# Performance work log

Hardware: AMD Instinct MI355X
Metric: run time of the kernel (lower is better)

The kernel has to match this reference:

```python
import jax, jax.numpy as jnp
import numpy as np

B, IN_CHAN, L = 16, 16, 4096
OUTC, KS = 64, 7

def _conv1d(x, w, b, stride=1, pad=0):
    # x: (N, Cin, L), w: (Cout, Cin, K)
    y = jax.lax.conv_general_dilated(x, w, (stride,), [(pad, pad)],
                                     dimension_numbers=('NCH', 'OIH', 'NCH'))
    return y + b[None, :, None]

def setup_inputs() -> dict:
    key = jax.random.key(0)
    ks = jax.random.split(key, 7)
    x = jax.random.normal(ks[0], (B, 1, L, IN_CHAN), dtype=jnp.float32)
    # offset-predicting conv (inc=1 -> KS offsets), k=3 pad=1
    p_w = jax.random.normal(ks[1], (KS, 1, 3), dtype=jnp.float32) * 0.1
    p_b = jax.random.normal(ks[2], (KS,), dtype=jnp.float32) * 0.1
    # modulation conv (inc=1 -> KS masks), k=3 pad=1
    m_w = jax.random.normal(ks[3], (KS, 1, 3), dtype=jnp.float32) * 0.1
    m_b = jax.random.normal(ks[4], (KS,), dtype=jnp.float32) * 0.1
    # main conv over resampled signal: (1 -> OUTC), k=KS, stride=KS
    c_w = jax.random.normal(ks[5], (OUTC, 1, KS), dtype=jnp.float32) * (1.0 / np.sqrt(KS))
    c_b = jax.random.normal(ks[6], (OUTC,), dtype=jnp.float32) * 0.1
    return {"x": x, "p_w": p_w, "p_b": p_b, "m_w": m_w, "m_b": m_b,
            "c_w": c_w, "c_b": c_b}

def _deform_conv1d(xs, p_w, p_b, m_w, m_b, c_w, c_b):
    # xs: (N, 1, L) single-channel 1D signal; returns (N, OUTC, L)
    N, _, Lx = xs.shape
    ksz = c_w.shape[2]
    offset = _conv1d(xs, p_w, p_b, pad=1)              # (N, ks, L)
    m = jax.nn.sigmoid(_conv1d(xs, m_w, m_b, pad=1))   # (N, ks, L)
    p_n = jnp.arange(-(ksz - 1) // 2, (ksz - 1) // 2 + 1, dtype=xs.dtype)  # kernel offsets
    p_0 = jnp.arange(1, Lx + 1, dtype=xs.dtype)        # base grid (starts at 1, as in deform-conv-v2)
    p = p_0[None, None, :] + p_n[None, :, None] + offset  # (N, ks, L)
    p = jnp.transpose(p, (0, 2, 1))                       # (N, L, ks)
    q_lt = jnp.clip(jnp.floor(jax.lax.stop_gradient(p)), 0, Lx - 1)
    q_rb = jnp.clip(q_lt + 1, 0, Lx - 1)
    p = jnp.clip(p, 0, Lx - 1)
    g_lt = 1 + (q_lt - p)                               # linear-interp weights
    g_rb = 1 - (q_rb - p)
    sig = xs[:, 0, :]                                   # (N, L) since inc == 1
    idx_lt = q_lt.astype(jnp.int32).reshape(N, Lx * ksz)
    idx_rb = q_rb.astype(jnp.int32).reshape(N, Lx * ksz)
    x_lt = jnp.take_along_axis(sig, idx_lt, axis=1).reshape(N, Lx, ksz)
    x_rb = jnp.take_along_axis(sig, idx_rb, axis=1).reshape(N, Lx, ksz)
    x_off = (g_lt * x_lt + g_rb * x_rb) * jnp.transpose(m, (0, 2, 1))  # (N, L, ks)
    x_off = x_off.reshape(N, 1, Lx * ksz)
    return _conv1d(x_off, c_w, c_b, stride=ksz)         # (N, OUTC, L)

def reference(x, p_w, p_b, m_w, m_b, c_w, c_b):
    # x: (B, 1, L, C); same DeformConv1D applied independently to every last-dim slice.
    # Fold the slice loop into the batch dim (same math, no Python loop).
    Bx, _, Lx, Cx = x.shape
    xs = jnp.transpose(x, (0, 3, 1, 2)).reshape(Bx * Cx, 1, Lx)
    y = _deform_conv1d(xs, p_w, p_b, m_w, m_b, c_w, c_b)  # (B*C, OUTC, L)
    y = y.reshape(Bx, Cx, -1, Lx)
    return jnp.transpose(y, (0, 2, 3, 1))                 # (B, OUTC, L, C)
```

## Files before the change

kernel.cpp:

```cpp
#include <hip/hip_runtime.h>
#include <math.h>

#define BB   16
#define CC   16
#define LL   4096
#define OUTC 64
#define KS   7

#define HALO 16
#define WIN  96
#define XST  17

typedef float vfloat4 __attribute__((ext_vector_type(4)));

__global__ __launch_bounds__(256) void deform_conv_kernel(
    const float* __restrict__ x,
    const float* __restrict__ p_w,
    const float* __restrict__ p_b,
    const float* __restrict__ m_w,
    const float* __restrict__ m_b,
    const float* __restrict__ c_w,
    const float* __restrict__ c_b,
    float* __restrict__ out)
{
    __shared__ float cw_lds[OUTC * 8];
    __shared__ float pw_lds[KS * 4];
    __shared__ float mw_lds[KS * 4];
    __shared__ float xs[WIN * XST];

    const int tid   = threadIdx.x;
    const int b     = blockIdx.x >> 6;
    const int ltile = blockIdx.x & 63;
    const int base  = ltile * 64 - HALO;

    const float* xb = x + b * (LL * CC);

    for (int i = tid; i < OUTC * 8; i += 256) {
        int o = i >> 3, j = i & 7;
        cw_lds[i] = (j < 7) ? c_w[o * 7 + j] : c_b[o];
    }
    if (tid < KS * 4) {
        int k = tid >> 2, j = tid & 3;
        pw_lds[tid] = (j < 3) ? p_w[k * 3 + j] : p_b[k];
        mw_lds[tid] = (j < 3) ? m_w[k * 3 + j] : m_b[k];
    }
    for (int i = tid; i < WIN * CC; i += 256) {
        int dpos = i >> 4;
        int c    = i & 15;
        int pos  = base + dpos;
        float v  = (pos >= 0 && pos < LL) ? xb[pos * CC + c] : 0.f;
        xs[dpos * XST + c] = v;
    }
    __syncthreads();

    const int cg = tid & 3;
    const int lo = tid >> 2;
    const int l  = ltile * 64 + lo;
    const int c0 = cg * 4;
    const int dl = lo + HALO;

    float s_m1[4], s_p1[4], s_0[4];
    #pragma unroll
    for (int c = 0; c < 4; ++c) {
        s_0[c]  = xs[dl * XST + c0 + c];
        s_m1[c] = (l > 0)      ? xs[(dl - 1) * XST + c0 + c] : 0.f;
        s_p1[c] = (l < LL - 1) ? xs[(dl + 1) * XST + c0 + c] : 0.f;
    }

    float xoff[4][KS];
    const float pl = (float)(l + 1);
    #pragma unroll
    for (int k = 0; k < KS; ++k) {
        float4 pw = *(const float4*)(pw_lds + k * 4);
        float4 mw = *(const float4*)(mw_lds + k * 4);
        const float pn = (float)(k - 3);
        #pragma unroll
        for (int c = 0; c < 4; ++c) {
            float off  = pw.w + pw.x * s_m1[c] + pw.y * s_0[c] + pw.z * s_p1[c];
            float mact = mw.w + mw.x * s_m1[c] + mw.y * s_0[c] + mw.z * s_p1[c];
            float mm   = 1.f / (1.f + __expf(-mact));

            float p    = pl + pn + off;
            float qltf = fminf(fmaxf(floorf(p), 0.f), (float)(LL - 1));
            float qrbf = fminf(qltf + 1.f, (float)(LL - 1));
            float pc   = fminf(fmaxf(p, 0.f), (float)(LL - 1));
            float glt  = 1.f + (qltf - pc);
            float grb  = 1.f - (qrbf - pc);

            int ilt = (int)qltf;
            int irb = (int)qrbf;
            int dlt = ilt - base;
            int drb = irb - base;
            int ci  = c0 + c;
            float xlt, xrb;
            if ((unsigned)dlt < WIN && (unsigned)drb < WIN) {
                xlt = xs[dlt * XST + ci];
                xrb = xs[drb * XST + ci];
            } else {
                xlt = xb[ilt * CC + ci];
                xrb = xb[irb * CC + ci];
            }
            xoff[c][k] = (glt * xlt + grb * xrb) * mm;
        }
    }

    float* outp = out + ((size_t)(b * OUTC) * LL + l) * CC + c0;
    #pragma unroll 4
    for (int o = 0; o < OUTC; ++o) {
        float4 w0 = *(const float4*)(cw_lds + o * 8);
        float4 w1 = *(const float4*)(cw_lds + o * 8 + 4);
        float acc[4];
        #pragma unroll
        for (int c = 0; c < 4; ++c) {
            float a = w1.w;
            a += w0.x * xoff[c][0];
            a += w0.y * xoff[c][1];
            a += w0.z * xoff[c][2];
            a += w0.w * xoff[c][3];
            a += w1.x * xoff[c][4];
            a += w1.y * xoff[c][5];
            a += w1.z * xoff[c][6];
            acc[c] = a;
        }
        vfloat4 res;
        res.x = acc[0]; res.y = acc[1]; res.z = acc[2]; res.w = acc[3];
        __builtin_nontemporal_store(res, (vfloat4*)(outp + (size_t)o * (LL * CC)));
    }
}

extern "C" void kernel_launch(void* const* d_in, const int* in_sizes, int n_in,
                              void* d_out, int out_size, void* d_ws, size_t ws_size,
                              hipStream_t stream) {
    const float* x   = (const float*)d_in[0];
    const float* p_w = (const float*)d_in[1];
    const float* p_b = (const float*)d_in[2];
    const float* m_w = (const float*)d_in[3];
    const float* m_b = (const float*)d_in[4];
    const float* c_w = (const float*)d_in[5];
    const float* c_b = (const float*)d_in[6];
    float* out = (float*)d_out;

    deform_conv_kernel<<<dim3(BB * 64), dim3(256), 0, stream>>>(
        x, p_w, p_b, m_w, m_b, c_w, c_b, out);
}
```

Baseline: 294.0 us.

## Split output channels across four blocks to raise grid parallelism

The grid grows fourfold by giving each block a quarter of the 64 output channels. The offset, mask and interpolation work is recomputed in every block. This gives more blocks to fill the MI355X's CUs, since 1024 blocks was a small grid. It also adds a launch-bounds occupancy hint of 8 blocks per CU, and the small weight loads are spread over different threads. The cost is fourfold redundant input loading and deform-sampling arithmetic.

Result: slower. 508.7 us (+73.0%).

```diff
diff --git a/kernel.cpp b/kernel.cpp
--- a/kernel.cpp
+++ b/kernel.cpp
@@ -7,13 +7,16 @@
 #define OUTC 64
 #define KS   7
 
+#define OSPLIT 4
+#define OPB    (OUTC / OSPLIT)
+
 #define HALO 16
 #define WIN  96
 #define XST  17
 
 typedef float vfloat4 __attribute__((ext_vector_type(4)));
 
-__global__ __launch_bounds__(256) void deform_conv_kernel(
+__global__ __launch_bounds__(256, 8) void deform_conv_kernel(
     const float* __restrict__ x,
     const float* __restrict__ p_w,
     const float* __restrict__ p_b,
@@ -23,33 +26,38 @@
     const float* __restrict__ c_b,
     float* __restrict__ out)
 {
-    __shared__ float cw_lds[OUTC * 8];
+    __shared__ float cw_lds[OPB * 8];
     __shared__ float pw_lds[KS * 4];
     __shared__ float mw_lds[KS * 4];
     __shared__ float xs[WIN * XST];
 
     const int tid   = threadIdx.x;
-    const int b     = blockIdx.x >> 6;
+    const int os    = blockIdx.x >> 10;
+    const int b     = (blockIdx.x >> 6) & 15;
     const int ltile = blockIdx.x & 63;
+    const int obase = os * OPB;
     const int base  = ltile * 64 - HALO;
 
     const float* xb = x + b * (LL * CC);
 
-    for (int i = tid; i < OUTC * 8; i += 256) {
-        int o = i >> 3, j = i & 7;
-        cw_lds[i] = (j < 7) ? c_w[o * 7 + j] : c_b[o];
+    if (tid < OPB * 8) {
+        int oi = tid >> 3, j = tid & 7;
+        int o  = obase + oi;
+        cw_lds[tid] = (j < 7) ? c_w[o * 7 + j] : c_b[o];
     }
-    if (tid < KS * 4) {
-        int k = tid >> 2, j = tid & 3;
-        pw_lds[tid] = (j < 3) ? p_w[k * 3 + j] : p_b[k];
-        mw_lds[tid] = (j < 3) ? m_w[k * 3 + j] : m_b[k];
+    if (tid >= 128 && tid < 128 + KS * 4) {
+        int t = tid - 128, k = t >> 2, j = t & 3;
+        pw_lds[t] = (j < 3) ? p_w[k * 3 + j] : p_b[k];
+    }
+    if (tid >= 192 && tid < 192 + KS * 4) {
+        int t = tid - 192, k = t >> 2, j = t & 3;
+        mw_lds[t] = (j < 3) ? m_w[k * 3 + j] : m_b[k];
     }
     for (int i = tid; i < WIN * CC; i += 256) {
         int dpos = i >> 4;
         int c    = i & 15;
         int pos  = base + dpos;
-        float v  = (pos >= 0 && pos < LL) ? xb[pos * CC + c] : 0.f;
-        xs[dpos * XST + c] = v;
+        xs[dpos * XST + c] = (pos >= 0 && pos < LL) ? xb[pos * CC + c] : 0.f;
     }
     __syncthreads();
 
@@ -104,11 +112,11 @@
         }
     }
 
-    float* outp = out + ((size_t)(b * OUTC) * LL + l) * CC + c0;
+    float* outp = out + (((size_t)b * OUTC + obase) * LL + l) * CC + c0;
     #pragma unroll 4
-    for (int o = 0; o < OUTC; ++o) {
-        float4 w0 = *(const float4*)(cw_lds + o * 8);
-        float4 w1 = *(const float4*)(cw_lds + o * 8 + 4);
+    for (int oi = 0; oi < OPB; ++oi) {
+        float4 w0 = *(const float4*)(cw_lds + oi * 8);
+        float4 w1 = *(const float4*)(cw_lds + oi * 8 + 4);
         float acc[4];
         #pragma unroll
         for (int c = 0; c < 4; ++c) {
@@ -124,7 +132,7 @@
         }
         vfloat4 res;
         res.x = acc[0]; res.y = acc[1]; res.z = acc[2]; res.w = acc[3];
-        __builtin_nontemporal_store(res, (vfloat4*)(outp + (size_t)o * (LL * CC)));
+        __builtin_nontemporal_store(res, (vfloat4*)(outp + (size_t)oi * (LL * CC)));
     }
 }
 
@@ -140,6 +148,6 @@
     const float* c_b = (const float*)d_in[6];
     float* out = (float*)d_out;
 
-    deform_conv_kernel<<<dim3(BB * 64), dim3(256), 0, stream>>>(
+    deform_conv_kernel<<<dim3(OSPLIT * BB * 64), dim3(256), 0, stream>>>(
         x, p_w, p_b, m_w, m_b, c_w, c_b, out);
 }
```
